# Optimization experiments

Measured on AMD Instinct MI355X. Metric: run time of the kernel, lower is better.

## Reference

```python
import jax, jax.numpy as jnp
import numpy as np

B, T, C, H, W = 2, 2, 128, 256, 256
PS = 8
N_HEAD = 1


def conv3(x, w, bias):
    # x: (N, C, H, W), w: (O, I, 3, 3) -> SAME 3x3 conv
    y = jax.lax.conv_general_dilated(x, w, (1, 1), 'SAME',
                                     dimension_numbers=('NCHW', 'OIHW', 'NCHW'))
    return y + bias[None, :, None, None]


def prelu(x, a):
    return jnp.where(x >= 0, x, a[0] * x)


def window_partition(x, k):
    # x: (B, T, H, W, C) -> (B*nH*nW, T, k, k, C)
    b, t, h, w, c = x.shape
    x = x.reshape(b, t, h // k, k, w // k, k, c)
    return x.transpose(0, 2, 4, 1, 3, 5, 6).reshape(-1, t, k, k, c)


def window_reverse(win, k, h, w):
    wb, t, _, _, c = win.shape
    b = wb // ((h // k) * (w // k))
    x = win.reshape(b, h // k, w // k, t, k, k, c)
    return x.transpose(0, 3, 1, 4, 2, 5, 6).reshape(b, t, h, w, c)


def mha(q, kv, n_head, scale):
    # q: (wb, nq, c), kv: (wb, nkv, c); K and V share the same tensor kv
    wb, nq, c = q.shape
    nkv = kv.shape[1]
    sc = c // n_head
    qh = q.reshape(wb, nq, n_head, sc).transpose(0, 2, 1, 3) * scale
    kvh = kv.reshape(wb, nkv, n_head, sc).transpose(0, 2, 1, 3)
    attn = jax.nn.softmax(jnp.einsum('bhqd,bhkd->bhqk', qh, kvh), axis=-1)
    x = jnp.einsum('bhqk,bhkd->bhqd', attn, kvh)
    return x.transpose(0, 2, 1, 3).reshape(wb, nq, c)


def setup_inputs() -> dict:
    key = jax.random.key(0)
    ks = jax.random.split(key, 12)
    f = lambda k, s: jax.random.normal(k, s, dtype=jnp.float32)
    return {
        'xq': f(ks[0], (B, C, H, W)),
        'xkvw': f(ks[1], (B * 2 * T, C, H, W)),
        'xkv': f(ks[2], (B * T, C, H, W)),
        'em': jax.random.uniform(ks[3], (B, 1, H, W), dtype=jnp.float32),
        'Wq': f(ks[4], (C, C, 3, 3)) * 0.05,
        'bq': f(ks[5], (C,)) * 0.05,
        'aq': jnp.full((1,), 0.25, jnp.float32),
        'Wkv': f(ks[6], (C, C, 3, 3)) * 0.05,
        'bkv': f(ks[7], (C,)) * 0.05,
        'akv': jnp.full((1,), 0.25, jnp.float32),
        'Wff': f(ks[8], (C, C, 3, 3)) * 0.05,
        'bff': f(ks[9], (C,)) * 0.05,
        'aff': jnp.full((1,), 0.25, jnp.float32),
        'b': B, 't': T, 'c': C,
    }


def reference(xq, xkvw, xkv, em, Wq, bq, aq, Wkv, bkv, akv, Wff, bff, aff, b, t, c):
    h, w = xq.shape[2], xq.shape[3]
    scale = c ** (-0.5)
    # residual conv embeddings (KV and KVw share the same embedding weights)
    Q = xq + prelu(conv3(xq, Wq, bq), aq)
    KV = xkv + prelu(conv3(xkv, Wkv, bkv), akv)
    KVw = xkvw + prelu(conv3(xkvw, Wkv, bkv), akv)
    shortcut = Q
    # to (b, T, h, w, c) layout
    Qs = Q.reshape(b, 1, c, h, w).transpose(0, 1, 3, 4, 2)
    KVws = KVw.reshape(b, 2 * t, c, h, w).transpose(0, 1, 3, 4, 2)
    KVs = KV.reshape(b, t, c, h, w).transpose(0, 1, 3, 4, 2)
    Masks = em.reshape(b, 1, 1, h, w).transpose(0, 1, 3, 4, 2)
    # windowing (shift=False -> no roll)
    Qw = window_partition(Qs, PS)
    wb = Qw.shape[0]
    Qw = Qw.reshape(wb, -1, c)
    KVs_w = window_partition(KVs, PS).reshape(wb, -1, c)
    KVws_w = window_partition(KVws, PS).reshape(wb, -1, c)
    Mw = window_partition(Masks, PS).reshape(wb, -1, 1)
    # mask-blended dual-branch windowed attention
    out = Mw * mha(Qw, KVs_w, N_HEAD, scale) + (1.0 - Mw) * mha(Qw, KVws_w, N_HEAD, scale)
    out = out.reshape(-1, 1, PS, PS, c)
    out = window_reverse(out, PS, h, w)  # (b, 1, h, w, c)
    Qo = shortcut + out.transpose(0, 1, 4, 2, 3).reshape(b, c, h, w)
    Qo = Qo + prelu(conv3(Qo, Wff, bff), aff)
    return Qo
```

## Files before the change

### kernel.cpp

```cpp
#include <hip/hip_runtime.h>


typedef unsigned short u16;
typedef __attribute__((ext_vector_type(8))) __bf16 bf16x8;
typedef __attribute__((ext_vector_type(4))) float f32x4;

union F4 { float4 v; float f[4]; };
union US4 { ushort4 s; u16 u[4]; };
union V16 { int4 i4; ushort4 s4[2]; u16 u[8]; };

__device__ __forceinline__ u16 f2b(float f) {
  union { float f; unsigned u; } c; c.f = f;
  unsigned r = c.u + 0x7fffu + ((c.u >> 16) & 1u);
  return (u16)(r >> 16);
}
__device__ __forceinline__ bf16x8 ld8(const u16* p) {
  union { ushort4 s[2]; bf16x8 v; } u;
  u.s[0] = *(const ushort4*)p;
  u.s[1] = *(const ushort4*)(p + 4);
  return u.v;
}

#define HW 65536

__global__ void prep_w(const float* __restrict__ W, u16* __restrict__ Wt) {
  int i = blockIdx.x * 256 + threadIdx.x;
  if (i >= 9 * 128 * 128) return;
  int s = i / 16384, rem = i % 16384;
  int o = rem >> 7, ci = rem & 127;
  Wt[i] = f2b(W[(o * 128 + ci) * 9 + s]);
}

__global__ __launch_bounds__(256, 2) void conv3x3_k(
    const float* __restrict__ X, const u16* __restrict__ Wt,
    const float* __restrict__ bias, const float* __restrict__ alpha,
    void* __restrict__ Out, int x_nhwc, int out_mode) {
  __shared__ __align__(16) char smem[44352];
  u16* in_t = (u16*)smem;
  u16* w_t = (u16*)(smem + 26928);
  float* o_t = (float*)smem;
  u16* ob_t = (u16*)smem;

  const int blk = blockIdx.x;
  const int xb = blk & 3, y = (blk >> 2) & 255, img = blk >> 10;
  const int x0 = xb * 64;
  const int tid = threadIdx.x;
  const int lane = tid & 63, wv = tid >> 6;
  const int quad = lane >> 4, l15 = lane & 15;

  f32x4 acc[2][4];
  const f32x4 zero4 = {0.f, 0.f, 0.f, 0.f};
#pragma unroll
  for (int i = 0; i < 2; ++i)
#pragma unroll
    for (int j = 0; j < 4; ++j) acc[i][j] = zero4;

  const float alf = alpha[0];

  for (int h = 0; h < 2; ++h) {
    __syncthreads();
    if (x_nhwc) {
      for (int i = tid; i < 3168; i += 256) {
        int r = i / 1056, rem = i % 1056, ix = rem >> 4, c4 = rem & 15;
        int yy = y - 1 + r, xx = x0 - 1 + ix;
        F4 v;
        if ((unsigned)yy < 256u && (unsigned)xx < 256u)
          v.v = *(const float4*)(X + (((img * 256 + yy) * 256 + xx) * 128 + h * 64 + c4 * 4));
        else
          v.v = (float4){0.f, 0.f, 0.f, 0.f};
        US4 s;
#pragma unroll
        for (int j = 0; j < 4; ++j) s.u[j] = f2b(v.f[j]);
        *(ushort4*)&in_t[(r * 66 + ix) * 68 + c4 * 4] = s.s;
      }
    } else {
      for (int i = tid; i < 3072; i += 256) {
        int c = i / 48, rem = i % 48, r = rem >> 4, c4 = rem & 15;
        int yy = y - 1 + r;
        F4 v;
        if ((unsigned)yy < 256u)
          v.v = *(const float4*)(X + ((img * 128 + h * 64 + c) * HW + yy * 256 + x0 + c4 * 4));
        else
          v.v = (float4){0.f, 0.f, 0.f, 0.f};
        int li = (r * 66 + 1 + c4 * 4) * 68 + c;
#pragma unroll
        for (int j = 0; j < 4; ++j) in_t[li + j * 68] = f2b(v.f[j]);
      }
      for (int i = tid; i < 384; i += 256) {
        int c = i / 6, rem = i % 6, r = rem >> 1, e = rem & 1;
        int yy = y - 1 + r;
        int xx = e ? (x0 + 64) : (x0 - 1);
        u16 val = 0;
        if ((unsigned)yy < 256u && (unsigned)xx < 256u)
          val = f2b(X[(img * 128 + h * 64 + c) * HW + yy * 256 + xx]);
        in_t[(r * 66 + (e ? 65 : 0)) * 68 + c] = val;
      }
    }
    __syncthreads();
    for (int s = 0; s < 9; ++s) {
      const int ky = s / 3, kx = s % 3;
      if (s) __syncthreads();
      for (int i = tid; i < 1024; i += 256) {
        int o = i >> 3, ch = i & 7;
        V16 v;
        v.i4 = *(const int4*)(Wt + (s * 16384 + o * 128 + h * 64 + ch * 8));
        int li = o * 68 + ch * 8;
        *(ushort4*)&w_t[li] = v.s4[0];
        *(ushort4*)&w_t[li + 4] = v.s4[1];
      }
      __syncthreads();
#pragma unroll
      for (int kb = 0; kb < 2; ++kb) {
        const int c0 = kb * 32 + quad * 8;
        bf16x8 a0 = ld8(&w_t[(wv * 32 + l15) * 68 + c0]);
        bf16x8 a1 = ld8(&w_t[(wv * 32 + 16 + l15) * 68 + c0]);
#pragma unroll
        for (int nt = 0; nt < 4; ++nt) {
          int ix = nt * 16 + l15 + kx;
          bf16x8 b = ld8(&in_t[(ky * 66 + ix) * 68 + c0]);
          acc[0][nt] = __builtin_amdgcn_mfma_f32_16x16x32_bf16(a0, b, acc[0][nt], 0, 0, 0);
          acc[1][nt] = __builtin_amdgcn_mfma_f32_16x16x32_bf16(a1, b, acc[1][nt], 0, 0, 0);
        }
      }
    }
  }
  __syncthreads();
  if (out_mode == 0) {
    float* Outf = (float*)Out;
#pragma unroll
    for (int mt = 0; mt < 2; ++mt)
#pragma unroll
      for (int nt = 0; nt < 4; ++nt)
#pragma unroll
        for (int r = 0; r < 4; ++r) {
          int ch = wv * 32 + mt * 16 + quad * 4 + r;
          int n = nt * 16 + l15;
          float xres = x_nhwc ? X[((img * 256 + y) * 256 + x0 + n) * 128 + ch]
                              : X[(img * 128 + ch) * HW + y * 256 + x0 + n];
          float v = acc[mt][nt][r] + bias[ch];
          v = v >= 0.f ? v : alf * v;
          Outf[(img * 128 + ch) * HW + y * 256 + x0 + n] = v + xres;
        }
  } else if (out_mode == 1) {
    float* Outf = (float*)Out;
#pragma unroll
    for (int mt = 0; mt < 2; ++mt)
#pragma unroll
      for (int nt = 0; nt < 4; ++nt)
#pragma unroll
        for (int r = 0; r < 4; ++r) {
          int ch = wv * 32 + mt * 16 + quad * 4 + r;
          int n = nt * 16 + l15;
          float xres = x_nhwc ? X[((img * 256 + y) * 256 + x0 + n) * 128 + ch]
                              : X[(img * 128 + ch) * HW + y * 256 + x0 + n];
          float v = acc[mt][nt][r] + bias[ch];
          v = v >= 0.f ? v : alf * v;
          o_t[n * 132 + ch] = v + xres;
        }
    __syncthreads();
    for (int i = tid; i < 2048; i += 256) {
      int px = i >> 5, c4 = i & 31;
      float4 v = *(const float4*)&o_t[px * 132 + c4 * 4];
      *(float4*)(Outf + (((img * 256 + y) * 256 + x0 + px) * 128 + c4 * 4)) = v;
    }
  } else {
    u16* Outb = (u16*)Out;
#pragma unroll
    for (int mt = 0; mt < 2; ++mt)
#pragma unroll
      for (int nt = 0; nt < 4; ++nt)
#pragma unroll
        for (int r = 0; r < 4; ++r) {
          int ch = wv * 32 + mt * 16 + quad * 4 + r;
          int n = nt * 16 + l15;
          float xres = x_nhwc ? X[((img * 256 + y) * 256 + x0 + n) * 128 + ch]
                              : X[(img * 128 + ch) * HW + y * 256 + x0 + n];
          float v = acc[mt][nt][r] + bias[ch];
          v = v >= 0.f ? v : alf * v;
          ob_t[n * 132 + ch] = f2b(v + xres);
        }
    __syncthreads();
    for (int i = tid; i < 1024; i += 256) {
      int px = i >> 4, c8 = i & 15;
      V16 v;
      v.s4[0] = *(const ushort4*)&ob_t[px * 132 + c8 * 8];
      v.s4[1] = *(const ushort4*)&ob_t[px * 132 + c8 * 8 + 4];
      *(int4*)(Outb + (((img * 256 + y) * 256 + x0 + px) * 128 + c8 * 8)) = v.i4;
    }
  }
}

#define ATT_SCALE 0.08838834764831845f
#define LOG2E 1.4426950408889634f

template <int NB>
__device__ __forceinline__ void attn_branch(
    const u16* __restrict__ kv, int b, int Y0, int X0,
    u16* kv_t, u16* p_t, const bf16x8 qf[4],
    int tid, int wv, int quad, int l15,
    f32x4 oacc[8], float lsum[4]) {
  f32x4 sacc[NB][4];
  const f32x4 zero4 = {0.f, 0.f, 0.f, 0.f};
#pragma unroll
  for (int i = 0; i < NB; ++i)
#pragma unroll
    for (int j = 0; j < 4; ++j) sacc[i][j] = zero4;

  for (int kb = 0; kb < NB; ++kb) {
    __syncthreads();
    for (int i = tid; i < 1024; i += 256) {
      int j = i >> 4, ch = i & 15;
      int yy = Y0 + (j >> 3), xx = X0 + (j & 7);
      int img = b * NB + kb;
      V16 v;
      v.i4 = *(const int4*)(kv + (((img * 256 + yy) * 256 + xx) * 128 + ch * 8));
      int li = j * 132 + ch * 8;
      *(ushort4*)&kv_t[li] = v.s4[0];
      *(ushort4*)&kv_t[li + 4] = v.s4[1];
    }
    __syncthreads();
#pragma unroll
    for (int kst = 0; kst < 4; ++kst) {
#pragma unroll
      for (int nt = 0; nt < 4; ++nt) {
        bf16x8 bk = ld8(&kv_t[(nt * 16 + l15) * 132 + kst * 32 + quad * 8]);
        sacc[kb][nt] = __builtin_amdgcn_mfma_f32_16x16x32_bf16(qf[kst], bk, sacc[kb][nt], 0, 0, 0);
      }
    }
  }
  float mx[4];
#pragma unroll
  for (int r = 0; r < 4; ++r) {
    float m = -1e30f;
#pragma unroll
    for (int kb = 0; kb < NB; ++kb)
#pragma unroll
      for (int nt = 0; nt < 4; ++nt) m = fmaxf(m, sacc[kb][nt][r]);
    for (int d = 1; d < 16; d <<= 1) m = fmaxf(m, __shfl_xor(m, d, 64));
    mx[r] = m * ATT_SCALE;
  }
#pragma unroll
  for (int r = 0; r < 4; ++r) {
    float s = 0.f;
#pragma unroll
    for (int kb = 0; kb < NB; ++kb)
#pragma unroll
      for (int nt = 0; nt < 4; ++nt) {
        float p = exp2f((sacc[kb][nt][r] * ATT_SCALE - mx[r]) * LOG2E);
        sacc[kb][nt][r] = p;
        s += p;
      }
    for (int d = 1; d < 16; d <<= 1) s += __shfl_xor(s, d, 64);
    lsum[r] = s;
  }
#pragma unroll
  for (int i = 0; i < 8; ++i) oacc[i] = zero4;
  for (int kb = 0; kb < NB; ++kb) {
    __syncthreads();
    for (int i = tid; i < 1024; i += 256) {
      int j = i >> 4, ch = i & 15;
      int yy = Y0 + (j >> 3), xx = X0 + (j & 7);
      int img = b * NB + kb;
      V16 v;
      v.i4 = *(const int4*)(kv + (((img * 256 + yy) * 256 + xx) * 128 + ch * 8));
#pragma unroll
      for (int cc = 0; cc < 8; ++cc) kv_t[(ch * 8 + cc) * 68 + j] = v.u[cc];
    }
#pragma unroll
    for (int nt = 0; nt < 4; ++nt)
#pragma unroll
      for (int r = 0; r < 4; ++r)
        p_t[(wv * 16 + quad * 4 + r) * 68 + nt * 16 + l15] = f2b(sacc[kb][nt][r]);
    __syncthreads();
#pragma unroll
    for (int kst = 0; kst < 2; ++kst) {
      bf16x8 ap = ld8(&p_t[(wv * 16 + l15) * 68 + kst * 32 + quad * 8]);
#pragma unroll
      for (int nt = 0; nt < 8; ++nt) {
        bf16x8 bv = ld8(&kv_t[(nt * 16 + l15) * 68 + kst * 32 + quad * 8]);
        oacc[nt] = __builtin_amdgcn_mfma_f32_16x16x32_bf16(ap, bv, oacc[nt], 0, 0, 0);
      }
    }
  }
}

__global__ __launch_bounds__(256, 2) void attn_k(
    float* __restrict__ Qn,
    const u16* __restrict__ KVn, const u16* __restrict__ KVwn,
    const float* __restrict__ em) {
  __shared__ __align__(16) u16 q_t[64 * 132];
  __shared__ __align__(16) u16 kv_t[128 * 68];
  __shared__ __align__(16) u16 p_t[64 * 68];

  const int wi = blockIdx.x;
  const int b = wi >> 10, wy = (wi >> 5) & 31, wx = wi & 31;
  const int Y0 = wy * 8, X0 = wx * 8;
  const int tid = threadIdx.x, lane = tid & 63, wv = tid >> 6;
  const int quad = lane >> 4, l15 = lane & 15;

  for (int i = tid; i < 2048; i += 256) {
    int qq = i >> 5, c4 = i & 31;
    int yy = Y0 + (qq >> 3), xx = X0 + (qq & 7);
    F4 v;
    v.v = *(const float4*)(Qn + (((b * 256 + yy) * 256 + xx) * 128 + c4 * 4));
    US4 s;
#pragma unroll
    for (int j = 0; j < 4; ++j) s.u[j] = f2b(v.f[j]);
    *(ushort4*)&q_t[qq * 132 + c4 * 4] = s.s;
  }
  float mval[4];
#pragma unroll
  for (int r = 0; r < 4; ++r) {
    int q = wv * 16 + quad * 4 + r;
    mval[r] = em[b * 65536 + (Y0 + (q >> 3)) * 256 + X0 + (q & 7)];
  }
  __syncthreads();
  bf16x8 qf[4];
#pragma unroll
  for (int kst = 0; kst < 4; ++kst)
    qf[kst] = ld8(&q_t[(wv * 16 + l15) * 132 + kst * 32 + quad * 8]);

  f32x4 o1[8], o2[8];
  float l1[4], l2[4];
  attn_branch<2>(KVn, b, Y0, X0, kv_t, p_t, qf, tid, wv, quad, l15, o1, l1);
  attn_branch<4>(KVwn, b, Y0, X0, kv_t, p_t, qf, tid, wv, quad, l15, o2, l2);

#pragma unroll
  for (int r = 0; r < 4; ++r) { l1[r] = 1.f / l1[r]; l2[r] = 1.f / l2[r]; }
#pragma unroll
  for (int nt = 0; nt < 8; ++nt) {
#pragma unroll
    for (int r = 0; r < 4; ++r) {
      int q = wv * 16 + quad * 4 + r;
      int c = nt * 16 + l15;
      int gi = ((b * 256 + Y0 + (q >> 3)) * 256 + X0 + (q & 7)) * 128 + c;
      float v = mval[r] * (o1[nt][r] * l1[r]) + (1.f - mval[r]) * (o2[nt][r] * l2[r]);
      v += Qn[gi];
      Qn[gi] = v;
    }
  }
}

extern "C" void kernel_launch(void* const* d_in, const int* in_sizes, int n_in,
                              void* d_out, int out_size, void* d_ws, size_t ws_size,
                              hipStream_t stream) {
  (void)in_sizes; (void)n_in; (void)out_size; (void)ws_size;
  const float* xq   = (const float*)d_in[0];
  const float* xkvw = (const float*)d_in[1];
  const float* xkv  = (const float*)d_in[2];
  const float* em   = (const float*)d_in[3];
  const float* Wq   = (const float*)d_in[4];
  const float* bq   = (const float*)d_in[5];
  const float* aq   = (const float*)d_in[6];
  const float* Wkv  = (const float*)d_in[7];
  const float* bkv  = (const float*)d_in[8];
  const float* akv  = (const float*)d_in[9];
  const float* Wff  = (const float*)d_in[10];
  const float* bff  = (const float*)d_in[11];
  const float* aff  = (const float*)d_in[12];

  char* ws = (char*)d_ws;
  float* Qn = (float*)ws;
  u16* KVn  = (u16*)(ws + 67108864);
  u16* KVwn = (u16*)(ws + 134217728);
  u16* wtq  = (u16*)d_out;
  u16* wtkv = (u16*)d_out + 147456;
  u16* wtff = KVwn;

  prep_w<<<576, 256, 0, stream>>>(Wq, wtq);
  prep_w<<<576, 256, 0, stream>>>(Wkv, wtkv);

  conv3x3_k<<<2048, 256, 0, stream>>>(xq,   wtq,  bq,  aq,  Qn,   0, 1);
  conv3x3_k<<<4096, 256, 0, stream>>>(xkv,  wtkv, bkv, akv, KVn,  0, 2);
  conv3x3_k<<<8192, 256, 0, stream>>>(xkvw, wtkv, bkv, akv, KVwn, 0, 2);

  attn_k<<<2048, 256, 0, stream>>>(Qn, KVn, KVwn, em);

  prep_w<<<576, 256, 0, stream>>>(Wff, wtff);
  conv3x3_k<<<2048, 256, 0, stream>>>(Qn, wtff, bff, aff, d_out, 1, 0);
}
```

Measured before the change: 1.658 ms.

## Tile conv over two output rows with XOR-swizzled LDS and 4x4 MFMA per wave

Each conv block now computes two output rows (64 px by 128 channels) instead of one. The 2x2 wave grid gives each wave 64 channels by one row, and each wave reuses 4 A and 4 B fragments across 16 MFMAs. Input and weight tiles move to an XOR-swizzled 128-byte-row LDS layout with 16-byte loads, and the NCHW input staging is rewritten to gather per pixel. Per-tap weight tile loads and input halo traffic are halved per output, at the cost of higher accumulator register pressure under a 3-blocks-per-CU launch bound, and strided channel gathers in the NCHW load path.

```diff
diff --git a/kernel.cpp b/kernel.cpp
--- a/kernel.cpp
+++ b/kernel.cpp
@@ -19,6 +19,14 @@
   u.s[0] = *(const ushort4*)p;
   u.s[1] = *(const ushort4*)(p + 4);
   return u.v;
+}
+__device__ __forceinline__ bf16x8 ld8b(const char* p) {
+  union { int4 i; bf16x8 v; } u;
+  u.i = *(const int4*)p;
+  return u.v;
+}
+__device__ __forceinline__ int swz(int row, int chunk) {
+  return row * 128 + (((chunk ^ row) & 7) << 4);
 }
 
 #define HW 65536
@@ -31,27 +39,28 @@
   Wt[i] = f2b(W[(o * 128 + ci) * 9 + s]);
 }
 
-__global__ __launch_bounds__(256, 2) void conv3x3_k(
+__global__ __launch_bounds__(256, 3) void conv3x3_k(
     const float* __restrict__ X, const u16* __restrict__ Wt,
     const float* __restrict__ bias, const float* __restrict__ alpha,
     void* __restrict__ Out, int x_nhwc, int out_mode) {
-  __shared__ __align__(16) char smem[44352];
-  u16* in_t = (u16*)smem;
-  u16* w_t = (u16*)(smem + 26928);
+  __shared__ __align__(16) char smem[50176];
+  char* inb = smem;
+  char* wb = smem + 33792;
   float* o_t = (float*)smem;
   u16* ob_t = (u16*)smem;
 
   const int blk = blockIdx.x;
-  const int xb = blk & 3, y = (blk >> 2) & 255, img = blk >> 10;
-  const int x0 = xb * 64;
+  const int xb = blk & 3, yb = (blk >> 2) & 127, img = blk >> 9;
+  const int x0 = xb * 64, y0 = yb * 2;
   const int tid = threadIdx.x;
   const int lane = tid & 63, wv = tid >> 6;
+  const int wr = wv >> 1, wc = wv & 1;
   const int quad = lane >> 4, l15 = lane & 15;
 
-  f32x4 acc[2][4];
+  f32x4 acc[4][4];
   const f32x4 zero4 = {0.f, 0.f, 0.f, 0.f};
 #pragma unroll
-  for (int i = 0; i < 2; ++i)
+  for (int i = 0; i < 4; ++i)
 #pragma unroll
     for (int j = 0; j < 4; ++j) acc[i][j] = zero4;
 
@@ -60,132 +69,152 @@
   for (int h = 0; h < 2; ++h) {
     __syncthreads();
     if (x_nhwc) {
-      for (int i = tid; i < 3168; i += 256) {
-        int r = i / 1056, rem = i % 1056, ix = rem >> 4, c4 = rem & 15;
-        int yy = y - 1 + r, xx = x0 - 1 + ix;
-        F4 v;
-        if ((unsigned)yy < 256u && (unsigned)xx < 256u)
-          v.v = *(const float4*)(X + (((img * 256 + yy) * 256 + xx) * 128 + h * 64 + c4 * 4));
-        else
-          v.v = (float4){0.f, 0.f, 0.f, 0.f};
-        US4 s;
-#pragma unroll
-        for (int j = 0; j < 4; ++j) s.u[j] = f2b(v.f[j]);
-        *(ushort4*)&in_t[(r * 66 + ix) * 68 + c4 * 4] = s.s;
+      for (int i = tid; i < 2112; i += 256) {
+        int e = i >> 3, c8 = i & 7;
+        int r = e / 66, ix = e - r * 66;
+        int yy = y0 - 1 + r, xx = x0 - 1 + ix;
+        V16 w;
+        if ((unsigned)yy < 256u && (unsigned)xx < 256u) {
+          const float* src = X + (((img * 256 + yy) * 256 + xx) * 128 + h * 64 + c8 * 8);
+          F4 a, b2;
+          a.v = *(const float4*)src;
+          b2.v = *(const float4*)(src + 4);
+#pragma unroll
+          for (int j = 0; j < 4; ++j) {
+            w.u[j] = f2b(a.f[j]);
+            w.u[4 + j] = f2b(b2.f[j]);
+          }
+        } else {
+          w.u[0] = 0; w.u[1] = 0; w.u[2] = 0; w.u[3] = 0;
+          w.u[4] = 0; w.u[5] = 0; w.u[6] = 0; w.u[7] = 0;
+        }
+        *(int4*)(inb + swz(e, c8)) = w.i4;
       }
     } else {
-      for (int i = tid; i < 3072; i += 256) {
-        int c = i / 48, rem = i % 48, r = rem >> 4, c4 = rem & 15;
-        int yy = y - 1 + r;
-        F4 v;
-        if ((unsigned)yy < 256u)
-          v.v = *(const float4*)(X + ((img * 128 + h * 64 + c) * HW + yy * 256 + x0 + c4 * 4));
-        else
-          v.v = (float4){0.f, 0.f, 0.f, 0.f};
-        int li = (r * 66 + 1 + c4 * 4) * 68 + c;
-#pragma unroll
-        for (int j = 0; j < 4; ++j) in_t[li + j * 68] = f2b(v.f[j]);
-      }
-      for (int i = tid; i < 384; i += 256) {
-        int c = i / 6, rem = i % 6, r = rem >> 1, e = rem & 1;
-        int yy = y - 1 + r;
-        int xx = e ? (x0 + 64) : (x0 - 1);
-        u16 val = 0;
-        if ((unsigned)yy < 256u && (unsigned)xx < 256u)
-          val = f2b(X[(img * 128 + h * 64 + c) * HW + yy * 256 + xx]);
-        in_t[(r * 66 + (e ? 65 : 0)) * 68 + c] = val;
-      }
-    }
-    __syncthreads();
+      for (int e = tid; e < 264; e += 256) {
+        int r = e / 66, ix = e - r * 66;
+        int yy = y0 - 1 + r, xx = x0 - 1 + ix;
+        if ((unsigned)yy < 256u && (unsigned)xx < 256u) {
+          const float* src = X + ((img * 128 + h * 64) * HW + yy * 256 + xx);
+#pragma unroll
+          for (int c8 = 0; c8 < 8; ++c8) {
+            V16 w;
+#pragma unroll
+            for (int cc = 0; cc < 8; ++cc)
+              w.u[cc] = f2b(src[(c8 * 8 + cc) * HW]);
+            *(int4*)(inb + swz(e, c8)) = w.i4;
+          }
+        } else {
+          V16 w;
+          w.u[0] = 0; w.u[1] = 0; w.u[2] = 0; w.u[3] = 0;
+          w.u[4] = 0; w.u[5] = 0; w.u[6] = 0; w.u[7] = 0;
+#pragma unroll
+          for (int c8 = 0; c8 < 8; ++c8)
+            *(int4*)(inb + swz(e, c8)) = w.i4;
+        }
+      }
+    }
     for (int s = 0; s < 9; ++s) {
-      const int ky = s / 3, kx = s % 3;
+      const int ky = s / 3, kx = s - ky * 3;
       if (s) __syncthreads();
       for (int i = tid; i < 1024; i += 256) {
-        int o = i >> 3, ch = i & 7;
-        V16 v;
-        v.i4 = *(const int4*)(Wt + (s * 16384 + o * 128 + h * 64 + ch * 8));
-        int li = o * 68 + ch * 8;
-        *(ushort4*)&w_t[li] = v.s4[0];
-        *(ushort4*)&w_t[li + 4] = v.s4[1];
+        int o = i >> 3, j = i & 7;
+        int4 v = *(const int4*)(Wt + (s * 16384 + o * 128 + h * 64 + j * 8));
+        *(int4*)(wb + swz(o, j)) = v;
       }
       __syncthreads();
 #pragma unroll
       for (int kb = 0; kb < 2; ++kb) {
-        const int c0 = kb * 32 + quad * 8;
-        bf16x8 a0 = ld8(&w_t[(wv * 32 + l15) * 68 + c0]);
-        bf16x8 a1 = ld8(&w_t[(wv * 32 + 16 + l15) * 68 + c0]);
+        bf16x8 af[4], bf[4];
+#pragma unroll
+        for (int mt = 0; mt < 4; ++mt)
+          af[mt] = ld8b(wb + swz(wr * 64 + mt * 16 + l15, kb * 4 + quad));
 #pragma unroll
         for (int nt = 0; nt < 4; ++nt) {
-          int ix = nt * 16 + l15 + kx;
-          bf16x8 b = ld8(&in_t[(ky * 66 + ix) * 68 + c0]);
-          acc[0][nt] = __builtin_amdgcn_mfma_f32_16x16x32_bf16(a0, b, acc[0][nt], 0, 0, 0);
-          acc[1][nt] = __builtin_amdgcn_mfma_f32_16x16x32_bf16(a1, b, acc[1][nt], 0, 0, 0);
+          int e = (wc + ky) * 66 + nt * 16 + l15 + kx;
+          bf[nt] = ld8b(inb + swz(e, kb * 4 + quad));
         }
+#pragma unroll
+        for (int mt = 0; mt < 4; ++mt)
+#pragma unroll
+          for (int nt = 0; nt < 4; ++nt)
+            acc[mt][nt] = __builtin_amdgcn_mfma_f32_16x16x32_bf16(af[mt], bf[nt], acc[mt][nt], 0, 0, 0);
       }
     }
   }
   __syncthreads();
   if (out_mode == 0) {
     float* Outf = (float*)Out;
-#pragma unroll
-    for (int mt = 0; mt < 2; ++mt)
+    const int yy = y0 + wc;
+#pragma unroll
+    for (int mt = 0; mt < 4; ++mt)
 #pragma unroll
       for (int nt = 0; nt < 4; ++nt)
 #pragma unroll
         for (int r = 0; r < 4; ++r) {
-          int ch = wv * 32 + mt * 16 + quad * 4 + r;
-          int n = nt * 16 + l15;
-          float xres = x_nhwc ? X[((img * 256 + y) * 256 + x0 + n) * 128 + ch]
-                              : X[(img * 128 + ch) * HW + y * 256 + x0 + n];
+          int ch = wr * 64 + mt * 16 + quad * 4 + r;
+          int x = nt * 16 + l15;
+          float xres = x_nhwc ? X[((img * 256 + yy) * 256 + x0 + x) * 128 + ch]
+                              : X[(img * 128 + ch) * HW + yy * 256 + x0 + x];
           float v = acc[mt][nt][r] + bias[ch];
           v = v >= 0.f ? v : alf * v;
-          Outf[(img * 128 + ch) * HW + y * 256 + x0 + n] = v + xres;
+          Outf[(img * 128 + ch) * HW + yy * 256 + x0 + x] = v + xres;
         }
   } else if (out_mode == 1) {
     float* Outf = (float*)Out;
-#pragma unroll
-    for (int mt = 0; mt < 2; ++mt)
-#pragma unroll
-      for (int nt = 0; nt < 4; ++nt)
-#pragma unroll
-        for (int r = 0; r < 4; ++r) {
-          int ch = wv * 32 + mt * 16 + quad * 4 + r;
-          int n = nt * 16 + l15;
-          float xres = x_nhwc ? X[((img * 256 + y) * 256 + x0 + n) * 128 + ch]
-                              : X[(img * 128 + ch) * HW + y * 256 + x0 + n];
-          float v = acc[mt][nt][r] + bias[ch];
-          v = v >= 0.f ? v : alf * v;
-          o_t[n * 132 + ch] = v + xres;
-        }
-    __syncthreads();
-    for (int i = tid; i < 2048; i += 256) {
-      int px = i >> 5, c4 = i & 31;
-      float4 v = *(const float4*)&o_t[px * 132 + c4 * 4];
-      *(float4*)(Outf + (((img * 256 + y) * 256 + x0 + px) * 128 + c4 * 4)) = v;
+    for (int ph = 0; ph < 2; ++ph) {
+      const int yy = y0 + ph;
+      if (ph) __syncthreads();
+      if (wc == ph) {
+#pragma unroll
+        for (int mt = 0; mt < 4; ++mt)
+#pragma unroll
+          for (int nt = 0; nt < 4; ++nt)
+#pragma unroll
+            for (int r = 0; r < 4; ++r) {
+              int ch = wr * 64 + mt * 16 + quad * 4 + r;
+              int x = nt * 16 + l15;
+              float xres = x_nhwc ? X[((img * 256 + yy) * 256 + x0 + x) * 128 + ch]
+                                  : X[(img * 128 + ch) * HW + yy * 256 + x0 + x];
+              float v = acc[mt][nt][r] + bias[ch];
+              v = v >= 0.f ? v : alf * v;
+              o_t[x * 132 + ch] = v + xres;
+            }
+      }
+      __syncthreads();
+      for (int i = tid; i < 2048; i += 256) {
+        int px = i >> 5, c4 = i & 31;
+        float4 v = *(const float4*)&o_t[px * 132 + c4 * 4];
+        *(float4*)(Outf + (((img * 256 + yy) * 256 + x0 + px) * 128 + c4 * 4)) = v;
+      }
     }
   } else {
     u16* Outb = (u16*)Out;
-#pragma unroll
-    for (int mt = 0; mt < 2; ++mt)
-#pragma unroll
-      for (int nt = 0; nt < 4; ++nt)
-#pragma unroll
-        for (int r = 0; r < 4; ++r) {
-          int ch = wv * 32 + mt * 16 + quad * 4 + r;
-          int n = nt * 16 + l15;
-          float xres = x_nhwc ? X[((img * 256 + y) * 256 + x0 + n) * 128 + ch]
-                              : X[(img * 128 + ch) * HW + y * 256 + x0 + n];
-          float v = acc[mt][nt][r] + bias[ch];
-          v = v >= 0.f ? v : alf * v;
-          ob_t[n * 132 + ch] = f2b(v + xres);
-        }
-    __syncthreads();
-    for (int i = tid; i < 1024; i += 256) {
-      int px = i >> 4, c8 = i & 15;
-      V16 v;
-      v.s4[0] = *(const ushort4*)&ob_t[px * 132 + c8 * 8];
-      v.s4[1] = *(const ushort4*)&ob_t[px * 132 + c8 * 8 + 4];
-      *(int4*)(Outb + (((img * 256 + y) * 256 + x0 + px) * 128 + c8 * 8)) = v.i4;
+    for (int ph = 0; ph < 2; ++ph) {
+      const int yy = y0 + ph;
+      if (ph) __syncthreads();
+      if (wc == ph) {
+#pragma unroll
+        for (int mt = 0; mt < 4; ++mt)
+#pragma unroll
+          for (int nt = 0; nt < 4; ++nt)
+#pragma unroll
+            for (int r = 0; r < 4; ++r) {
+              int ch = wr * 64 + mt * 16 + quad * 4 + r;
+              int x = nt * 16 + l15;
+              float xres = x_nhwc ? X[((img * 256 + yy) * 256 + x0 + x) * 128 + ch]
+                                  : X[(img * 128 + ch) * HW + yy * 256 + x0 + x];
+              float v = acc[mt][nt][r] + bias[ch];
+              v = v >= 0.f ? v : alf * v;
+              ob_t[x * 136 + ch] = f2b(v + xres);
+            }
+      }
+      __syncthreads();
+      for (int i = tid; i < 1024; i += 256) {
+        int px = i >> 4, c8 = i & 15;
+        int4 v = *(const int4*)&ob_t[px * 136 + c8 * 8];
+        *(int4*)(Outb + (((img * 256 + yy) * 256 + x0 + px) * 128 + c8 * 8)) = v;
+      }
     }
   }
 }
@@ -370,12 +399,12 @@
   prep_w<<<576, 256, 0, stream>>>(Wq, wtq);
   prep_w<<<576, 256, 0, stream>>>(Wkv, wtkv);
 
-  conv3x3_k<<<2048, 256, 0, stream>>>(xq,   wtq,  bq,  aq,  Qn,   0, 1);
-  conv3x3_k<<<4096, 256, 0, stream>>>(xkv,  wtkv, bkv, akv, KVn,  0, 2);
-  conv3x3_k<<<8192, 256, 0, stream>>>(xkvw, wtkv, bkv, akv, KVwn, 0, 2);
+  conv3x3_k<<<1024, 256, 0, stream>>>(xq,   wtq,  bq,  aq,  Qn,   0, 1);
+  conv3x3_k<<<2048, 256, 0, stream>>>(xkv,  wtkv, bkv, akv, KVn,  0, 2);
+  conv3x3_k<<<4096, 256, 0, stream>>>(xkvw, wtkv, bkv, akv, KVwn, 0, 2);
 
   attn_k<<<2048, 256, 0, stream>>>(Qn, KVn, KVwn, em);
 
   prep_w<<<576, 256, 0, stream>>>(Wff, wtff);
-  conv3x3_k<<<2048, 256, 0, stream>>>(Qn, wtff, bff, aff, d_out, 1, 0);
-}
+  conv3x3_k<<<1024, 256, 0, stream>>>(Qn, wtff, bff, aff, d_out, 1, 0);
+}
```

After: 1.461 ms. 1.14x faster.
